# Kernel tuning notes

Measured on AMD Instinct MI355X. Metric: run time of the kernel, lower is better.

The kernel has to match this reference:

```python
import jax, jax.numpy as jnp
import numpy as np

B, F, K, D = 512, 2048, 64, 16


def setup_inputs() -> dict:
    key = jax.random.key(0)
    k1, k2 = jax.random.split(key)
    x = jax.random.normal(k1, (B, F), dtype=jnp.float32)
    # glorot-uniform-ish init for the projection kernel [F, K, D]
    limit = np.sqrt(6.0 / (F + K * D)).astype(np.float32)
    kernel = jax.random.uniform(k2, (F, K, D), dtype=jnp.float32, minval=-limit, maxval=limit)
    return {"x": x, "kernel": kernel}


def reference(x, kernel):
    # activation: [B, K, D]
    act = jnp.einsum('bf,fkd->bkd', x, kernel)
    # pairwise L1 distance over D: diffs [B, K, D, B] -> abs_diffs [B, K, B]
    diffs = act[:, :, :, None] - jnp.transpose(act, (1, 2, 0))[None, :, :, :]
    abs_diffs = jnp.sum(jnp.abs(diffs), axis=2)
    # exp-similarity summed over the other batch elements (includes self: +1)
    feats = jnp.sum(jnp.exp(-abs_diffs), axis=2)  # [B, K]
    return jnp.concatenate([x, feats], axis=1)  # [B, F + K]
```

## Files before the change

kernel.cpp:

```cpp
#include <hip/hip_runtime.h>
#include <hip/hip_fp16.h>

#define B_   512
#define F_   2048
#define K_   64
#define D_   16
#define N_   1024
#define OUTW (F_+K_)
#define LOG2E 1.44269504088896340736f
#define KSPLIT 4
#define KCH  (F_/KSPLIT)
#define BK   64
#define NSTEP (KCH/BK)

typedef __attribute__((ext_vector_type(8))) short short8;
typedef __attribute__((ext_vector_type(4))) float f32x4;

__device__ __forceinline__ ushort f2bf(float f) {
    union { float f; unsigned u; } un; un.f = f;
    unsigned u = un.u;
    u += 0x7FFF + ((u >> 16) & 1);
    return (ushort)(u >> 16);
}

__device__ __forceinline__ float exp2_neg(float x) {
    float r;
    asm("v_exp_f32 %0, -%1" : "=v"(r) : "v"(x));
    return r;
}

__global__ __launch_bounds__(256) void prep_kernel(const float* __restrict__ x,
                                                   const float* __restrict__ w,
                                                   float* __restrict__ out,
                                                   ushort* __restrict__ xb,
                                                   ushort* __restrict__ wt) {
    __shared__ float t[32][33];
    const int blk = blockIdx.x;
    const int tid = threadIdx.x;
    if (blk < 1024) {
        const int i = blk * 256 + tid;
        float4 v = ((const float4*)x)[i];
        const int b = i >> 9, c = i & 511;
        ((float4*)out)[b * (OUTW / 4) + c] = v;
        ushort4 u = make_ushort4(f2bf(v.x * LOG2E), f2bf(v.y * LOG2E),
                                 f2bf(v.z * LOG2E), f2bf(v.w * LOG2E));
        ((ushort4*)xb)[i] = u;
    } else {
        const int r  = tid >> 3;
        const int c4 = (tid & 7) * 4;
        #pragma unroll 1
        for (int i = 0; i < 8; ++i) {
            const int tb = (blk - 1024) * 8 + i;
            const int f0 = (tb >> 5) * 32, n0 = (tb & 31) * 32;
            float4 v = *(const float4*)(w + (size_t)(f0 + r) * N_ + n0 + c4);
            __syncthreads();
            t[r][c4 + 0] = v.x; t[r][c4 + 1] = v.y;
            t[r][c4 + 2] = v.z; t[r][c4 + 3] = v.w;
            __syncthreads();
            ushort4 u = make_ushort4(f2bf(t[c4 + 0][r]), f2bf(t[c4 + 1][r]),
                                     f2bf(t[c4 + 2][r]), f2bf(t[c4 + 3][r]));
            *(ushort4*)(wt + (size_t)(n0 + r) * F_ + f0 + c4) = u;
        }
    }
}

__global__ __launch_bounds__(256) void gemm_mfma_kernel(const ushort* __restrict__ xb,
                                                        const ushort* __restrict__ wt,
                                                        float* __restrict__ act) {
    __shared__ ushort As[2][64 * 64];
    __shared__ ushort Bs[2][64 * 64];

    const int bm0 = blockIdx.x * 64;
    const int bn0 = blockIdx.y * 64;
    const int f0  = blockIdx.z * KCH;
    const int tid = threadIdx.x;
    const int l   = tid & 63;
    const int w   = tid >> 6;
    const int mw  = (w >> 1) * 32;
    const int nw  = (w & 1) * 32;
    const int lr  = l & 15;
    const int lkc = l >> 4;
    const int sw  = lr & 7;

    const int r0 = tid >> 2;
    const int c0 = (tid & 3) * 2;
    const int c1 = c0 + 1;
    const ushort* gA0 = xb + (size_t)(bm0 + r0) * F_ + f0 + c0 * 8;
    const ushort* gA1 = gA0 + 8;
    const ushort* gB0 = wt + (size_t)(bn0 + r0) * F_ + f0 + c0 * 8;
    const ushort* gB1 = gB0 + 8;
    const int wA0 = r0 * 64 + ((c0 ^ (r0 & 7)) * 8);
    const int wA1 = r0 * 64 + ((c1 ^ (r0 & 7)) * 8);

    f32x4 acc00 = {}, acc01 = {}, acc10 = {}, acc11 = {};

    uint4 a0v = *(const uint4*)gA0;
    uint4 a1v = *(const uint4*)gA1;
    uint4 b0v = *(const uint4*)gB0;
    uint4 b1v = *(const uint4*)gB1;
    *(uint4*)&As[0][wA0] = a0v; *(uint4*)&As[0][wA1] = a1v;
    *(uint4*)&Bs[0][wA0] = b0v; *(uint4*)&Bs[0][wA1] = b1v;
    __syncthreads();

    #pragma unroll
    for (int s = 0; s < NSTEP; ++s) {
        const int cur = s & 1, nxt = cur ^ 1;
        if (s < NSTEP - 1) {
            a0v = *(const uint4*)(gA0 + (s + 1) * BK);
            a1v = *(const uint4*)(gA1 + (s + 1) * BK);
            b0v = *(const uint4*)(gB0 + (s + 1) * BK);
            b1v = *(const uint4*)(gB1 + (s + 1) * BK);
        }
        #pragma unroll
        for (int ks = 0; ks < 2; ++ks) {
            const int cb = ks * 4 + lkc;
            short8 a_0 = *(const short8*)&As[cur][(mw + lr) * 64      + ((cb ^ sw) * 8)];
            short8 a_1 = *(const short8*)&As[cur][(mw + 16 + lr) * 64 + ((cb ^ sw) * 8)];
            short8 b_0 = *(const short8*)&Bs[cur][(nw + lr) * 64      + ((cb ^ sw) * 8)];
            short8 b_1 = *(const short8*)&Bs[cur][(nw + 16 + lr) * 64 + ((cb ^ sw) * 8)];
            acc00 = __builtin_amdgcn_mfma_f32_16x16x32_bf16(a_0, b_0, acc00, 0, 0, 0);
            acc01 = __builtin_amdgcn_mfma_f32_16x16x32_bf16(a_0, b_1, acc01, 0, 0, 0);
            acc10 = __builtin_amdgcn_mfma_f32_16x16x32_bf16(a_1, b_0, acc10, 0, 0, 0);
            acc11 = __builtin_amdgcn_mfma_f32_16x16x32_bf16(a_1, b_1, acc11, 0, 0, 0);
        }
        if (s < NSTEP - 1) {
            *(uint4*)&As[nxt][wA0] = a0v; *(uint4*)&As[nxt][wA1] = a1v;
            *(uint4*)&Bs[nxt][wA0] = b0v; *(uint4*)&Bs[nxt][wA1] = b1v;
        }
        __syncthreads();
    }

    #pragma unroll
    for (int mi = 0; mi < 2; ++mi) {
        #pragma unroll
        for (int ni = 0; ni < 2; ++ni) {
            const f32x4 a = (mi == 0) ? (ni == 0 ? acc00 : acc01)
                                      : (ni == 0 ? acc10 : acc11);
            const int n = bn0 + nw + ni * 16 + lr;
            const int k = n >> 4, d = n & 15;
            const int mbase = bm0 + mw + mi * 16 + lkc * 4;
            float* dst = act + ((size_t)k * B_ + mbase) * D_ + d;
            #pragma unroll
            for (int r = 0; r < 4; ++r)
                atomicAdd(dst + r * D_, a[r]);
        }
    }
}

__global__ __launch_bounds__(512) void pairwise_kernel(const float* __restrict__ act,
                                                       float* __restrict__ out) {
    __shared__ __half2 s2[B_ * D_ / 2];
    __shared__ float red[8][64];

    const int bt = blockIdx.x;
    const int k  = blockIdx.y;
    const int tid  = threadIdx.x;
    const int lane = tid & 63;
    const int wave = tid >> 6;

    const f32x4* src = (const f32x4*)(act + (size_t)k * (B_ * D_));
    #pragma unroll
    for (int i = 0; i < 4; ++i) {
        const int idx = tid + i * 512;
        f32x4 v = src[idx];
        s2[idx * 2]     = __floats2half2_rn(v[0], v[1]);
        s2[idx * 2 + 1] = __floats2half2_rn(v[2], v[3]);
    }
    const int b = bt * 64 + lane;
    __half2 ar[8];
    {
        const f32x4* arow = (const f32x4*)(act + ((size_t)k * B_ + b) * D_);
        #pragma unroll
        for (int i = 0; i < 4; ++i) {
            f32x4 v = arow[i];
            ar[i * 2]     = __floats2half2_rn(v[0], v[1]);
            ar[i * 2 + 1] = __floats2half2_rn(v[2], v[3]);
        }
    }
    __syncthreads();

    float p = 0.0f;
    const int b2lo = wave * 64;
    #pragma unroll 4
    for (int b2 = b2lo; b2 < b2lo + 64; ++b2) {
        const __half2* vr = &s2[b2 * 8];
        __half2 sA = __habs2(__hsub2(ar[0], vr[0]));
        __half2 sB = __habs2(__hsub2(ar[1], vr[1]));
        sA = __hadd2(sA, __habs2(__hsub2(ar[2], vr[2])));
        sB = __hadd2(sB, __habs2(__hsub2(ar[3], vr[3])));
        sA = __hadd2(sA, __habs2(__hsub2(ar[4], vr[4])));
        sB = __hadd2(sB, __habs2(__hsub2(ar[5], vr[5])));
        sA = __hadd2(sA, __habs2(__hsub2(ar[6], vr[6])));
        sB = __hadd2(sB, __habs2(__hsub2(ar[7], vr[7])));
        sA = __hadd2(sA, sB);
        const float dist = __low2float(sA) + __high2float(sA);
        p += exp2_neg(dist);
    }

    red[wave][lane] = p;
    __syncthreads();
    if (wave == 0) {
        float total = 0.0f;
        #pragma unroll
        for (int i = 0; i < 8; ++i) total += red[i][lane];
        out[(size_t)b * OUTW + F_ + k] = total;
    }
}

extern "C" void kernel_launch(void* const* d_in, const int* in_sizes, int n_in,
                              void* d_out, int out_size, void* d_ws, size_t ws_size,
                              hipStream_t stream) {
    const float* x = (const float*)d_in[0];
    const float* wsrc = (const float*)d_in[1];
    float* out = (float*)d_out;

    ushort* xb  = (ushort*)d_ws;
    ushort* wt  = (ushort*)((char*)d_ws + (size_t)2 * 1024 * 1024);
    float*  act = (float*)((char*)d_ws + (size_t)6 * 1024 * 1024);

    hipMemsetAsync(act, 0, (size_t)K_ * B_ * D_ * sizeof(float), stream);
    prep_kernel<<<1280, 256, 0, stream>>>(x, wsrc, out, xb, wt);
    gemm_mfma_kernel<<<dim3(8, 16, KSPLIT), 256, 0, stream>>>(xb, wt, act);
    pairwise_kernel<<<dim3(8, K_), 512, 0, stream>>>(act, out);
}
```

Before: 103.2 us.

## Fuse x conversion and copy into GEMM, replace atomics with split-K partial buffers

The x-to-bf16 conversion and the copy of x into the output move into the GEMM kernel, which now reads fp32 x directly and converts it while staging tiles in shared memory. The by==0 blocks write the x passthrough. Split-K results go to four separate partial buffers with plain stores instead of atomics, so the memset is no longer needed and the pairwise kernel sums the partials on load. Block indices are remapped for locality. This removes a launch, a memset, the xb round trip and atomic traffic, but each GEMM block now reads fp32 x at twice the bytes and redoes the conversion across the 16 N-blocks.

```diff
diff --git a/kernel.cpp b/kernel.cpp
--- a/kernel.cpp
+++ b/kernel.cpp
@@ -12,6 +12,7 @@
 #define KCH  (F_/KSPLIT)
 #define BK   64
 #define NSTEP (KCH/BK)
+#define KBD  (K_*B_*D_)
 
 typedef __attribute__((ext_vector_type(8))) short short8;
 typedef __attribute__((ext_vector_type(4))) float f32x4;
@@ -22,114 +23,123 @@
     u += 0x7FFF + ((u >> 16) & 1);
     return (ushort)(u >> 16);
 }
-
+__device__ __forceinline__ uint f2bf2(float lo, float hi) {
+    return (uint)f2bf(lo) | ((uint)f2bf(hi) << 16);
+}
 __device__ __forceinline__ float exp2_neg(float x) {
     float r;
     asm("v_exp_f32 %0, -%1" : "=v"(r) : "v"(x));
     return r;
 }
 
-__global__ __launch_bounds__(256) void prep_kernel(const float* __restrict__ x,
-                                                   const float* __restrict__ w,
-                                                   float* __restrict__ out,
-                                                   ushort* __restrict__ xb,
-                                                   ushort* __restrict__ wt) {
+__global__ __launch_bounds__(256) void prep_w_kernel(const float* __restrict__ w,
+                                                     ushort* __restrict__ wt) {
     __shared__ float t[32][33];
-    const int blk = blockIdx.x;
     const int tid = threadIdx.x;
-    if (blk < 1024) {
-        const int i = blk * 256 + tid;
-        float4 v = ((const float4*)x)[i];
-        const int b = i >> 9, c = i & 511;
-        ((float4*)out)[b * (OUTW / 4) + c] = v;
-        ushort4 u = make_ushort4(f2bf(v.x * LOG2E), f2bf(v.y * LOG2E),
-                                 f2bf(v.z * LOG2E), f2bf(v.w * LOG2E));
-        ((ushort4*)xb)[i] = u;
-    } else {
-        const int r  = tid >> 3;
-        const int c4 = (tid & 7) * 4;
-        #pragma unroll 1
-        for (int i = 0; i < 8; ++i) {
-            const int tb = (blk - 1024) * 8 + i;
-            const int f0 = (tb >> 5) * 32, n0 = (tb & 31) * 32;
-            float4 v = *(const float4*)(w + (size_t)(f0 + r) * N_ + n0 + c4);
-            __syncthreads();
-            t[r][c4 + 0] = v.x; t[r][c4 + 1] = v.y;
-            t[r][c4 + 2] = v.z; t[r][c4 + 3] = v.w;
-            __syncthreads();
-            ushort4 u = make_ushort4(f2bf(t[c4 + 0][r]), f2bf(t[c4 + 1][r]),
-                                     f2bf(t[c4 + 2][r]), f2bf(t[c4 + 3][r]));
-            *(ushort4*)(wt + (size_t)(n0 + r) * F_ + f0 + c4) = u;
-        }
-    }
-}
-
-__global__ __launch_bounds__(256) void gemm_mfma_kernel(const ushort* __restrict__ xb,
-                                                        const ushort* __restrict__ wt,
-                                                        float* __restrict__ act) {
+    const int r  = tid >> 3;
+    const int c4 = (tid & 7) * 4;
+    #pragma unroll 1
+    for (int i = 0; i < 8; ++i) {
+        const int tb = blockIdx.x * 8 + i;
+        const int f0 = (tb >> 5) * 32, n0 = (tb & 31) * 32;
+        float4 v = *(const float4*)(w + (size_t)(f0 + r) * N_ + n0 + c4);
+        __syncthreads();
+        t[r][c4 + 0] = v.x; t[r][c4 + 1] = v.y;
+        t[r][c4 + 2] = v.z; t[r][c4 + 3] = v.w;
+        __syncthreads();
+        ushort4 u = make_ushort4(f2bf(t[c4 + 0][r]), f2bf(t[c4 + 1][r]),
+                                 f2bf(t[c4 + 2][r]), f2bf(t[c4 + 3][r]));
+        *(ushort4*)(wt + (size_t)(n0 + r) * F_ + f0 + c4) = u;
+    }
+}
+
+__global__ __launch_bounds__(256) void gemm_fused_kernel(const float* __restrict__ x,
+                                                         const ushort* __restrict__ wt,
+                                                         float* __restrict__ out,
+                                                         float* __restrict__ actp) {
     __shared__ ushort As[2][64 * 64];
     __shared__ ushort Bs[2][64 * 64];
 
-    const int bm0 = blockIdx.x * 64;
-    const int bn0 = blockIdx.y * 64;
-    const int f0  = blockIdx.z * KCH;
+    const int flat = blockIdx.x;
+    const int wg = (flat & 7) * 64 + (flat >> 3);
+    const int bx = wg & 7, by = (wg >> 3) & 15, bz = wg >> 7;
+    const int bm0 = bx * 64, bn0 = by * 64, f0 = bz * KCH;
+
     const int tid = threadIdx.x;
-    const int l   = tid & 63;
-    const int w   = tid >> 6;
-    const int mw  = (w >> 1) * 32;
-    const int nw  = (w & 1) * 32;
-    const int lr  = l & 15;
-    const int lkc = l >> 4;
-    const int sw  = lr & 7;
-
-    const int r0 = tid >> 2;
+    const int l = tid & 63, wv = tid >> 6;
+    const int mw = (wv >> 1) * 32, nw = (wv & 1) * 32;
+    const int lr = l & 15, lkc = l >> 4, sw = lr & 7;
+
+    const int ar = tid >> 2, acg = tid & 3;
+    const f32x4* gA = (const f32x4*)(x + (size_t)(bm0 + ar) * F_ + f0) + acg * 4;
+    float* oA = out + (size_t)(bm0 + ar) * OUTW + f0 + acg * 16;
+    const int wa0 = ar * 64 + (((acg * 2)     ^ (ar & 7)) * 8);
+    const int wa1 = ar * 64 + (((acg * 2 + 1) ^ (ar & 7)) * 8);
     const int c0 = (tid & 3) * 2;
-    const int c1 = c0 + 1;
-    const ushort* gA0 = xb + (size_t)(bm0 + r0) * F_ + f0 + c0 * 8;
-    const ushort* gA1 = gA0 + 8;
-    const ushort* gB0 = wt + (size_t)(bn0 + r0) * F_ + f0 + c0 * 8;
+    const ushort* gB0 = wt + (size_t)(bn0 + ar) * F_ + f0 + c0 * 8;
     const ushort* gB1 = gB0 + 8;
-    const int wA0 = r0 * 64 + ((c0 ^ (r0 & 7)) * 8);
-    const int wA1 = r0 * 64 + ((c1 ^ (r0 & 7)) * 8);
-
-    f32x4 acc00 = {}, acc01 = {}, acc10 = {}, acc11 = {};
-
-    uint4 a0v = *(const uint4*)gA0;
-    uint4 a1v = *(const uint4*)gA1;
+    const int wb0 = ar * 64 + ((c0       ^ (ar & 7)) * 8);
+    const int wb1 = ar * 64 + (((c0 + 1) ^ (ar & 7)) * 8);
+
+    f32x4 a0r = gA[0], a1r = gA[1], a2r = gA[2], a3r = gA[3];
     uint4 b0v = *(const uint4*)gB0;
     uint4 b1v = *(const uint4*)gB1;
-    *(uint4*)&As[0][wA0] = a0v; *(uint4*)&As[0][wA1] = a1v;
-    *(uint4*)&Bs[0][wA0] = b0v; *(uint4*)&Bs[0][wA1] = b1v;
+
+    f32x4 acc00 = {}, acc01 = {}, acc10 = {}, acc11 = {};
+
+    {
+        uint4 ca = make_uint4(f2bf2(a0r[0]*LOG2E, a0r[1]*LOG2E), f2bf2(a0r[2]*LOG2E, a0r[3]*LOG2E),
+                              f2bf2(a1r[0]*LOG2E, a1r[1]*LOG2E), f2bf2(a1r[2]*LOG2E, a1r[3]*LOG2E));
+        uint4 cb = make_uint4(f2bf2(a2r[0]*LOG2E, a2r[1]*LOG2E), f2bf2(a2r[2]*LOG2E, a2r[3]*LOG2E),
+                              f2bf2(a3r[0]*LOG2E, a3r[1]*LOG2E), f2bf2(a3r[2]*LOG2E, a3r[3]*LOG2E));
+        *(uint4*)&As[0][wa0] = ca;  *(uint4*)&As[0][wa1] = cb;
+        *(uint4*)&Bs[0][wb0] = b0v; *(uint4*)&Bs[0][wb1] = b1v;
+        if (by == 0) {
+            *(f32x4*)(oA + 0)  = a0r; *(f32x4*)(oA + 4)  = a1r;
+            *(f32x4*)(oA + 8)  = a2r; *(f32x4*)(oA + 12) = a3r;
+        }
+    }
     __syncthreads();
 
     #pragma unroll
     for (int s = 0; s < NSTEP; ++s) {
-        const int cur = s & 1, nxt = cur ^ 1;
+        const int cur = s & 1;
         if (s < NSTEP - 1) {
-            a0v = *(const uint4*)(gA0 + (s + 1) * BK);
-            a1v = *(const uint4*)(gA1 + (s + 1) * BK);
+            a0r = gA[(s + 1) * 16 + 0]; a1r = gA[(s + 1) * 16 + 1];
+            a2r = gA[(s + 1) * 16 + 2]; a3r = gA[(s + 1) * 16 + 3];
             b0v = *(const uint4*)(gB0 + (s + 1) * BK);
             b1v = *(const uint4*)(gB1 + (s + 1) * BK);
         }
         #pragma unroll
         for (int ks = 0; ks < 2; ++ks) {
-            const int cb = ks * 4 + lkc;
-            short8 a_0 = *(const short8*)&As[cur][(mw + lr) * 64      + ((cb ^ sw) * 8)];
-            short8 a_1 = *(const short8*)&As[cur][(mw + 16 + lr) * 64 + ((cb ^ sw) * 8)];
-            short8 b_0 = *(const short8*)&Bs[cur][(nw + lr) * 64      + ((cb ^ sw) * 8)];
-            short8 b_1 = *(const short8*)&Bs[cur][(nw + 16 + lr) * 64 + ((cb ^ sw) * 8)];
-            acc00 = __builtin_amdgcn_mfma_f32_16x16x32_bf16(a_0, b_0, acc00, 0, 0, 0);
-            acc01 = __builtin_amdgcn_mfma_f32_16x16x32_bf16(a_0, b_1, acc01, 0, 0, 0);
-            acc10 = __builtin_amdgcn_mfma_f32_16x16x32_bf16(a_1, b_0, acc10, 0, 0, 0);
-            acc11 = __builtin_amdgcn_mfma_f32_16x16x32_bf16(a_1, b_1, acc11, 0, 0, 0);
+            const int cb_ = ks * 4 + lkc;
+            short8 A0 = *(const short8*)&As[cur][(mw + lr) * 64      + ((cb_ ^ sw) * 8)];
+            short8 A1 = *(const short8*)&As[cur][(mw + 16 + lr) * 64 + ((cb_ ^ sw) * 8)];
+            short8 B0 = *(const short8*)&Bs[cur][(nw + lr) * 64      + ((cb_ ^ sw) * 8)];
+            short8 B1 = *(const short8*)&Bs[cur][(nw + 16 + lr) * 64 + ((cb_ ^ sw) * 8)];
+            acc00 = __builtin_amdgcn_mfma_f32_16x16x32_bf16(A0, B0, acc00, 0, 0, 0);
+            acc01 = __builtin_amdgcn_mfma_f32_16x16x32_bf16(A0, B1, acc01, 0, 0, 0);
+            acc10 = __builtin_amdgcn_mfma_f32_16x16x32_bf16(A1, B0, acc10, 0, 0, 0);
+            acc11 = __builtin_amdgcn_mfma_f32_16x16x32_bf16(A1, B1, acc11, 0, 0, 0);
         }
         if (s < NSTEP - 1) {
-            *(uint4*)&As[nxt][wA0] = a0v; *(uint4*)&As[nxt][wA1] = a1v;
-            *(uint4*)&Bs[nxt][wA0] = b0v; *(uint4*)&Bs[nxt][wA1] = b1v;
+            const int nxt = cur ^ 1;
+            uint4 ca = make_uint4(f2bf2(a0r[0]*LOG2E, a0r[1]*LOG2E), f2bf2(a0r[2]*LOG2E, a0r[3]*LOG2E),
+                                  f2bf2(a1r[0]*LOG2E, a1r[1]*LOG2E), f2bf2(a1r[2]*LOG2E, a1r[3]*LOG2E));
+            uint4 cb = make_uint4(f2bf2(a2r[0]*LOG2E, a2r[1]*LOG2E), f2bf2(a2r[2]*LOG2E, a2r[3]*LOG2E),
+                                  f2bf2(a3r[0]*LOG2E, a3r[1]*LOG2E), f2bf2(a3r[2]*LOG2E, a3r[3]*LOG2E));
+            *(uint4*)&As[nxt][wa0] = ca;  *(uint4*)&As[nxt][wa1] = cb;
+            *(uint4*)&Bs[nxt][wb0] = b0v; *(uint4*)&Bs[nxt][wb1] = b1v;
+            if (by == 0) {
+                float* o = oA + (s + 1) * BK;
+                *(f32x4*)(o + 0) = a0r; *(f32x4*)(o + 4)  = a1r;
+                *(f32x4*)(o + 8) = a2r; *(f32x4*)(o + 12) = a3r;
+            }
         }
         __syncthreads();
     }
 
+    float* base = actp + (size_t)bz * KBD;
     #pragma unroll
     for (int mi = 0; mi < 2; ++mi) {
         #pragma unroll
@@ -138,16 +148,16 @@
                                       : (ni == 0 ? acc10 : acc11);
             const int n = bn0 + nw + ni * 16 + lr;
             const int k = n >> 4, d = n & 15;
-            const int mbase = bm0 + mw + mi * 16 + lkc * 4;
-            float* dst = act + ((size_t)k * B_ + mbase) * D_ + d;
+            const int mb = bm0 + mw + mi * 16 + lkc * 4;
+            float* dst = base + ((size_t)k * B_ + mb) * D_ + d;
             #pragma unroll
-            for (int r = 0; r < 4; ++r)
-                atomicAdd(dst + r * D_, a[r]);
-        }
-    }
-}
-
-__global__ __launch_bounds__(512) void pairwise_kernel(const float* __restrict__ act,
+            for (int r2 = 0; r2 < 4; ++r2)
+                dst[r2 * D_] = a[r2];
+        }
+    }
+}
+
+__global__ __launch_bounds__(512) void pairwise_kernel(const float* __restrict__ actp,
                                                        float* __restrict__ out) {
     __shared__ __half2 s2[B_ * D_ / 2];
     __shared__ float red[8][64];
@@ -158,24 +168,25 @@
     const int lane = tid & 63;
     const int wave = tid >> 6;
 
-    const f32x4* src = (const f32x4*)(act + (size_t)k * (B_ * D_));
+    const f32x4* p0 = (const f32x4*)(actp + (size_t)k * (B_ * D_));
+    const f32x4* p1 = p0 + KBD / 4;
+    const f32x4* p2 = p1 + KBD / 4;
+    const f32x4* p3 = p2 + KBD / 4;
     #pragma unroll
     for (int i = 0; i < 4; ++i) {
         const int idx = tid + i * 512;
-        f32x4 v = src[idx];
+        f32x4 v = (p0[idx] + p1[idx]) + (p2[idx] + p3[idx]);
         s2[idx * 2]     = __floats2half2_rn(v[0], v[1]);
         s2[idx * 2 + 1] = __floats2half2_rn(v[2], v[3]);
     }
     const int b = bt * 64 + lane;
-    __half2 ar[8];
-    {
-        const f32x4* arow = (const f32x4*)(act + ((size_t)k * B_ + b) * D_);
-        #pragma unroll
-        for (int i = 0; i < 4; ++i) {
-            f32x4 v = arow[i];
-            ar[i * 2]     = __floats2half2_rn(v[0], v[1]);
-            ar[i * 2 + 1] = __floats2half2_rn(v[2], v[3]);
-        }
+    __half2 arr[8];
+    #pragma unroll
+    for (int i = 0; i < 4; ++i) {
+        const int idx = b * 4 + i;
+        f32x4 v = (p0[idx] + p1[idx]) + (p2[idx] + p3[idx]);
+        arr[i * 2]     = __floats2half2_rn(v[0], v[1]);
+        arr[i * 2 + 1] = __floats2half2_rn(v[2], v[3]);
     }
     __syncthreads();
 
@@ -184,14 +195,14 @@
     #pragma unroll 4
     for (int b2 = b2lo; b2 < b2lo + 64; ++b2) {
         const __half2* vr = &s2[b2 * 8];
-        __half2 sA = __habs2(__hsub2(ar[0], vr[0]));
-        __half2 sB = __habs2(__hsub2(ar[1], vr[1]));
-        sA = __hadd2(sA, __habs2(__hsub2(ar[2], vr[2])));
-        sB = __hadd2(sB, __habs2(__hsub2(ar[3], vr[3])));
-        sA = __hadd2(sA, __habs2(__hsub2(ar[4], vr[4])));
-        sB = __hadd2(sB, __habs2(__hsub2(ar[5], vr[5])));
-        sA = __hadd2(sA, __habs2(__hsub2(ar[6], vr[6])));
-        sB = __hadd2(sB, __habs2(__hsub2(ar[7], vr[7])));
+        __half2 sA = __habs2(__hsub2(arr[0], vr[0]));
+        __half2 sB = __habs2(__hsub2(arr[1], vr[1]));
+        sA = __hadd2(sA, __habs2(__hsub2(arr[2], vr[2])));
+        sB = __hadd2(sB, __habs2(__hsub2(arr[3], vr[3])));
+        sA = __hadd2(sA, __habs2(__hsub2(arr[4], vr[4])));
+        sB = __hadd2(sB, __habs2(__hsub2(arr[5], vr[5])));
+        sA = __hadd2(sA, __habs2(__hsub2(arr[6], vr[6])));
+        sB = __hadd2(sB, __habs2(__hsub2(arr[7], vr[7])));
         sA = __hadd2(sA, sB);
         const float dist = __low2float(sA) + __high2float(sA);
         p += exp2_neg(dist);
@@ -214,12 +225,10 @@
     const float* wsrc = (const float*)d_in[1];
     float* out = (float*)d_out;
 
-    ushort* xb  = (ushort*)d_ws;
-    ushort* wt  = (ushort*)((char*)d_ws + (size_t)2 * 1024 * 1024);
-    float*  act = (float*)((char*)d_ws + (size_t)6 * 1024 * 1024);
-
-    hipMemsetAsync(act, 0, (size_t)K_ * B_ * D_ * sizeof(float), stream);
-    prep_kernel<<<1280, 256, 0, stream>>>(x, wsrc, out, xb, wt);
-    gemm_mfma_kernel<<<dim3(8, 16, KSPLIT), 256, 0, stream>>>(xb, wt, act);
-    pairwise_kernel<<<dim3(8, K_), 512, 0, stream>>>(act, out);
-}
+    ushort* wt   = (ushort*)d_ws;
+    float*  actp = (float*)((char*)d_ws + (size_t)4 * 1024 * 1024);
+
+    prep_w_kernel<<<256, 256, 0, stream>>>(wsrc, wt);
+    gemm_fused_kernel<<<512, 256, 0, stream>>>(x, wt, out, actp);
+    pairwise_kernel<<<dim3(8, K_), 512, 0, stream>>>(actp, out);
+}
```

Result: slower. 106.0 us (+2.7%).
